# Optimization experiments

Hardware: AMD Instinct MI355X
Metric: run time of the kernel (lower is better)

Reference implementation:

```python
import jax, jax.numpy as jnp
import numpy as np

B = 64          # number of batch items (segments)
L = 16          # tokens per header unit
IS = 1024       # hidden size iS
LENS = np.arange(B, dtype=np.int32) + 32   # ragged l_hs: 32..95, sum=4064, max=95
T = int(LENS.sum())
MAXL = int(LENS.max())
EPS = 1e-12


def setup_inputs() -> dict:
    key = jax.random.key(0)
    ks = jax.random.split(key, 5)
    s_is = 1.0 / np.sqrt(IS)
    s_2is = 1.0 / np.sqrt(2 * IS)
    return {
        "ctx": jax.random.normal(ks[0], (B, IS), jnp.float32),
        "wemb_hpu": jax.random.normal(ks[1], (T, L, IS), jnp.float32),
        "l_hpu": jnp.full((T,), L, dtype=jnp.int32),   # unused by forward (kept for signature parity)
        "l_hs": jnp.asarray(LENS),
        "max_l": MAXL,
        "U_w": jax.random.normal(ks[2], (IS, IS), jnp.float32) * s_is,
        "U_b": jnp.zeros((IS,), jnp.float32),
        "V_w": jax.random.normal(ks[3], (IS, IS), jnp.float32) * s_is,
        "V_b": jnp.zeros((IS,), jnp.float32),
        "enc_w": jax.random.normal(ks[4], (IS, 2 * IS), jnp.float32) * s_2is,
        "enc_b": jnp.zeros((IS,), jnp.float32),
        "gamma": jnp.ones((IS,), jnp.float32),
        "beta": jnp.zeros((IS,), jnp.float32),
    }


def reference(ctx, wemb_hpu, l_hpu, l_hs, max_l, U_w, U_b, V_w, V_b, enc_w, enc_b, gamma, beta):
    Bn, iS = ctx.shape
    Tn = wemb_hpu.shape[0]
    # map each of the T ragged rows to its batch segment b, and its position within the segment
    seg = jnp.repeat(jnp.arange(Bn), l_hs, total_repeat_length=Tn)          # [T]
    offs = jnp.concatenate([jnp.zeros((1,), l_hs.dtype), jnp.cumsum(l_hs)[:-1]])
    pos = jnp.arange(Tn) - offs[seg]                                        # [T]

    wenc_u = ctx @ U_w.T + U_b                                              # [B, iS]
    wenc_v = wemb_hpu @ V_w.T + V_b                                         # [T, L, iS]
    # attn = softmax over L of sum_d( U(ctx)[b] * V(wenc) )
    scores = jnp.einsum('tld,td->tl', wenc_v, wenc_u[seg])                  # [T, L]
    attn = jax.nn.softmax(scores, axis=-1)
    pooled = jnp.einsum('tl,tld->td', attn, wemb_hpu)                       # [T, iS]
    h = jnp.concatenate([pooled, ctx[seg]], axis=-1) @ enc_w.T + enc_b      # [T, iS]

    # scatter ragged rows into zero-padded [B, max_l, iS]
    padded = jnp.zeros((Bn, max_l, iS), h.dtype).at[seg, pos].set(h)

    # TF-style LayerNorm over last dim (applied to padding too, as in original)
    u = padded.mean(-1, keepdims=True)
    s2 = ((padded - u) ** 2).mean(-1, keepdims=True)
    return gamma * (padded - u) / jnp.sqrt(s2 + EPS) + beta
```

## Files before the change

kernel.cpp:

```cpp
#include <hip/hip_runtime.h>

typedef unsigned short u16;
typedef unsigned int u32;
typedef __attribute__((ext_vector_type(8))) short s16x8;
typedef __attribute__((ext_vector_type(4))) float f32x4;

#define IS_ 1024
#define LTOK 16

__device__ __forceinline__ u16 f2bf(float f) {
  u32 u = __builtin_bit_cast(u32, f);
  u32 r = (u + 0x7FFFu + ((u >> 16) & 1u)) >> 16;
  return (u16)r;
}

__device__ __forceinline__ float dot4(const float4& a, const float4& b) {
  return a.x * b.x + a.y * b.y + a.z * b.z + a.w * b.w;
}

__global__ void k_pre0(const int* __restrict__ l_hs, int* __restrict__ offs,
                       int* __restrict__ seg, int Bn, int Tn, int Mp) {
  __shared__ int so[65];
  const int tid = threadIdx.x;
  if (tid < 64) {
    int v = (tid < Bn) ? l_hs[tid] : 0;
#pragma unroll
    for (int off = 1; off < 64; off <<= 1) {
      int up = __shfl_up(v, off, 64);
      if (tid >= off) v += up;
    }
    so[tid + 1] = v;
    if (tid == 0) so[0] = 0;
  }
  __syncthreads();
  if (tid < 65) offs[tid] = so[tid];
  for (int t = tid; t < Mp; t += 256) {
    int s = 0;
    if (t < Tn) {
      int lo = 0, hi = Bn;
      while (hi - lo > 1) {
        int mid = (lo + hi) >> 1;
        if (so[mid] <= t) lo = mid; else hi = mid;
      }
      s = lo;
    }
    seg[t] = s;
  }
}

__global__ __launch_bounds__(256) void k_convW1(const float* __restrict__ enc_w,
                                                u16* __restrict__ W1) {
  const int i = blockIdx.x * 1024 + threadIdx.x * 4;
  const int r = i >> 10, k = i & 1023;
  float4 v = *(const float4*)&enc_w[(size_t)r * 2048 + k];
  uint2 pk;
  pk.x = (u32)f2bf(v.x) | ((u32)f2bf(v.y) << 16);
  pk.y = (u32)f2bf(v.z) | ((u32)f2bf(v.w) << 16);
  *(uint2*)&W1[i] = pk;
}

__global__ __launch_bounds__(256) void k_rowdot(const float* __restrict__ x,
                                                const float* __restrict__ W,
                                                const float* __restrict__ bias,
                                                float* __restrict__ outp,
                                                int ldW, int colOff) {
  __shared__ float cs[2][IS_];
  const int tid = threadIdx.x;
  const int b0 = blockIdx.y * 2;
  const int d = blockIdx.x * 256 + tid;
#pragma unroll
  for (int i = 0; i < 8; ++i) {
    int idx = i * 256 + tid;
    cs[idx >> 10][idx & 1023] = x[(b0 + (idx >> 10)) * IS_ + (idx & 1023)];
  }
  __syncthreads();
  float a0 = bias[d];
  float a1 = a0;
  const float* wr = W + (size_t)d * ldW + colOff;
#pragma unroll 4
  for (int e = 0; e < IS_; e += 4) {
    float4 w4 = *(const float4*)(wr + e);
    float4 c0 = *(const float4*)&cs[0][e];
    float4 c1 = *(const float4*)&cs[1][e];
    a0 += dot4(w4, c0);
    a1 += dot4(w4, c1);
  }
  outp[b0 * IS_ + d] = a0;
  outp[(b0 + 1) * IS_ + d] = a1;
}

__global__ __launch_bounds__(256) void k_preQ(const float* __restrict__ wencu,
                                              const float* __restrict__ Vw,
                                              float* __restrict__ q2) {
  __shared__ float us[2][IS_];
  const int tid = threadIdx.x;
  const int b0 = blockIdx.y * 2;
  const int e = blockIdx.x * 256 + tid;
#pragma unroll
  for (int i = 0; i < 8; ++i) {
    int idx = i * 256 + tid;
    us[idx >> 10][idx & 1023] = wencu[(b0 + (idx >> 10)) * IS_ + (idx & 1023)];
  }
  __syncthreads();
  float a0 = 0.f, a1 = 0.f;
#pragma unroll 2
  for (int dd = 0; dd < IS_; dd += 4) {
    float4 u0 = *(const float4*)&us[0][dd];
    float4 u1 = *(const float4*)&us[1][dd];
    float v0 = Vw[(size_t)(dd + 0) * IS_ + e];
    float v1 = Vw[(size_t)(dd + 1) * IS_ + e];
    float v2 = Vw[(size_t)(dd + 2) * IS_ + e];
    float v3 = Vw[(size_t)(dd + 3) * IS_ + e];
    a0 += u0.x * v0 + u0.y * v1 + u0.z * v2 + u0.w * v3;
    a1 += u1.x * v0 + u1.y * v1 + u1.z * v2 + u1.w * v3;
  }
  q2[b0 * IS_ + e] = a0;
  q2[(b0 + 1) * IS_ + e] = a1;
}

__global__ __launch_bounds__(256) void k_attn(const float* __restrict__ wemb,
                                              const float* __restrict__ q2,
                                              const int* __restrict__ seg,
                                              u16* __restrict__ pooled, int Tn) {
  const int t = blockIdx.x;
  const int tid = threadIdx.x;
  const int d4 = tid * 4;
  if (t >= Tn) {
    uint2 z; z.x = 0u; z.y = 0u;
    *(uint2*)&pooled[(size_t)t * IS_ + d4] = z;
    return;
  }
  const int b = seg[t];
  float4 q = *(const float4*)&q2[b * IS_ + d4];
  float4 w[LTOK];
  const float* base = wemb + (size_t)t * (LTOK * IS_) + d4;
#pragma unroll
  for (int l = 0; l < LTOK; ++l) w[l] = *(const float4*)(base + l * IS_);
  float s[LTOK];
#pragma unroll
  for (int l = 0; l < LTOK; ++l) s[l] = dot4(w[l], q);
#pragma unroll
  for (int l = 0; l < LTOK; ++l) {
#pragma unroll
    for (int m = 1; m < 64; m <<= 1) s[l] += __shfl_xor(s[l], m, 64);
  }
  __shared__ float sred[4][LTOK];
  const int wave = tid >> 6, lane = tid & 63;
  if (lane == 0) {
#pragma unroll
    for (int l = 0; l < LTOK; ++l) sred[wave][l] = s[l];
  }
  __syncthreads();
  float sc[LTOK];
#pragma unroll
  for (int l = 0; l < LTOK; ++l)
    sc[l] = sred[0][l] + sred[1][l] + sred[2][l] + sred[3][l];
  float mx = sc[0];
#pragma unroll
  for (int l = 1; l < LTOK; ++l) mx = fmaxf(mx, sc[l]);
  float den = 0.f;
#pragma unroll
  for (int l = 0; l < LTOK; ++l) { sc[l] = __expf(sc[l] - mx); den += sc[l]; }
  const float inv = 1.f / den;
  float px = 0.f, py = 0.f, pz = 0.f, pw = 0.f;
#pragma unroll
  for (int l = 0; l < LTOK; ++l) {
    float a = sc[l] * inv;
    px += a * w[l].x; py += a * w[l].y; pz += a * w[l].z; pw += a * w[l].w;
  }
  uint2 pk;
  pk.x = (u32)f2bf(px) | ((u32)f2bf(py) << 16);
  pk.y = (u32)f2bf(pz) | ((u32)f2bf(pw) << 16);
  *(uint2*)&pooled[(size_t)t * IS_ + d4] = pk;
}

__device__ __forceinline__ void gl2lds16(const void* g, void* l) {
  __builtin_amdgcn_global_load_lds(
      (const __attribute__((address_space(1))) u32*)g,
      (__attribute__((address_space(3))) u32*)l, 16, 0, 0);
}

__global__ __launch_bounds__(256) void k_gemm(const u16* __restrict__ A,
                                              const u16* __restrict__ B,
                                              float* __restrict__ C) {
  __shared__ __align__(16) u16 As[128 * 64];
  __shared__ __align__(16) u16 Bs[128 * 64];
  const int tid = threadIdx.x;
  const int wave = tid >> 6, lane = tid & 63;
  const int m0 = blockIdx.x * 128, n0 = blockIdx.y * 128;
  const int wm = (wave & 1) * 64, wn = (wave >> 1) * 64;
  f32x4 acc[4][4] = {};
  for (int kt = 0; kt < 1024; kt += 64) {
#pragma unroll
    for (int c = 0; c < 4; ++c) {
      int idx = c * 256 + tid;
      int row = idx >> 3;
      int kk = (idx & 7) * 8;
      gl2lds16(A + (size_t)(m0 + row) * 1024 + kt + kk, &As[idx * 8]);
      gl2lds16(B + (size_t)(n0 + row) * 1024 + kt + kk, &Bs[idx * 8]);
    }
    __syncthreads();
#pragma unroll
    for (int ks = 0; ks < 2; ++ks) {
      const int kb = ks * 32 + (lane >> 4) * 8;
      const int rr = lane & 15;
      s16x8 af[4], bf[4];
#pragma unroll
      for (int i = 0; i < 4; ++i) {
        af[i] = *(const s16x8*)&As[(wm + i * 16 + rr) * 64 + kb];
        bf[i] = *(const s16x8*)&Bs[(wn + i * 16 + rr) * 64 + kb];
      }
#pragma unroll
      for (int i = 0; i < 4; ++i)
#pragma unroll
        for (int j = 0; j < 4; ++j)
          acc[i][j] = __builtin_amdgcn_mfma_f32_16x16x32_bf16(af[i], bf[j], acc[i][j], 0, 0, 0);
    }
    __syncthreads();
  }
  const int col = lane & 15, rq = (lane >> 4) * 4;
#pragma unroll
  for (int i = 0; i < 4; ++i)
#pragma unroll
    for (int j = 0; j < 4; ++j) {
#pragma unroll
      for (int r = 0; r < 4; ++r)
        C[(size_t)(m0 + wm + i * 16 + rq + r) * 1024 + (n0 + wn + j * 16 + col)] = acc[i][j][r];
    }
}

__global__ __launch_bounds__(256) void k_ln(const float* __restrict__ h,
                                            const float* __restrict__ h2,
                                            const int* __restrict__ offs,
                                            const int* __restrict__ l_hs,
                                            const float* __restrict__ gamma,
                                            const float* __restrict__ beta,
                                            float* __restrict__ out, int maxL) {
  const int row = blockIdx.x;
  const int b = row / maxL, pos = row % maxL;
  const int tid = threadIdx.x, d4 = tid * 4;
  float4 be = *(const float4*)&beta[d4];
  float* orow = out + (size_t)row * IS_;
  if (pos >= l_hs[b]) {
    *(float4*)(orow + d4) = be;
    return;
  }
  const int t = offs[b] + pos;
  float4 x = *(const float4*)&h[(size_t)t * IS_ + d4];
  float4 y2 = *(const float4*)&h2[b * IS_ + d4];
  x.x += y2.x; x.y += y2.y; x.z += y2.z; x.w += y2.w;
  float s1 = x.x + x.y + x.z + x.w;
  float s2 = x.x * x.x + x.y * x.y + x.z * x.z + x.w * x.w;
#pragma unroll
  for (int m = 1; m < 64; m <<= 1) {
    s1 += __shfl_xor(s1, m, 64);
    s2 += __shfl_xor(s2, m, 64);
  }
  __shared__ float red[4][2];
  const int wave = tid >> 6, lane = tid & 63;
  if (lane == 0) { red[wave][0] = s1; red[wave][1] = s2; }
  __syncthreads();
  float S1 = red[0][0] + red[1][0] + red[2][0] + red[3][0];
  float S2 = red[0][1] + red[1][1] + red[2][1] + red[3][1];
  const float u = S1 * (1.f / 1024.f);
  const float var = S2 * (1.f / 1024.f) - u * u;
  const float rstd = rsqrtf(var + 1e-12f);
  float4 g = *(const float4*)&gamma[d4];
  float4 o;
  o.x = g.x * (x.x - u) * rstd + be.x;
  o.y = g.y * (x.y - u) * rstd + be.y;
  o.z = g.z * (x.z - u) * rstd + be.z;
  o.w = g.w * (x.w - u) * rstd + be.w;
  *(float4*)(orow + d4) = o;
}

extern "C" void kernel_launch(void* const* d_in, const int* in_sizes, int n_in,
                              void* d_out, int out_size, void* d_ws, size_t ws_size,
                              hipStream_t stream) {
  const float* ctx   = (const float*)d_in[0];
  const float* wemb  = (const float*)d_in[1];
  const int*   l_hs  = (const int*)d_in[3];
  const float* U_w   = (const float*)d_in[5];
  const float* U_b   = (const float*)d_in[6];
  const float* V_w   = (const float*)d_in[7];
  const float* enc_w = (const float*)d_in[9];
  const float* enc_b = (const float*)d_in[10];
  const float* gamma = (const float*)d_in[11];
  const float* beta  = (const float*)d_in[12];
  float* out = (float*)d_out;

  const int Bn = in_sizes[0] / IS_;
  const int Tn = in_sizes[1] / (LTOK * IS_);
  const int maxL = out_size / (Bn * IS_);
  const int Mp = (Tn + 127) & ~127;

  char* ws = (char*)d_ws;
  int*   offs   = (int*)(ws + 0x0);
  int*   seg    = (int*)(ws + 0x400);
  float* wencu  = (float*)(ws + 0x10000);
  float* q2     = (float*)(ws + 0x50000);
  float* h2     = (float*)(ws + 0x90000);
  u16*   W1     = (u16*)(ws + 0xD0000);
  u16*   pooled = (u16*)(ws + 0x2D0000);
  float* h      = (float*)(ws + 0xAD0000);

  k_pre0<<<1, 256, 0, stream>>>(l_hs, offs, seg, Bn, Tn, Mp);
  k_convW1<<<1024, 256, 0, stream>>>(enc_w, W1);
  k_rowdot<<<dim3(4, Bn / 2), 256, 0, stream>>>(ctx, U_w, U_b, wencu, 1024, 0);
  k_rowdot<<<dim3(4, Bn / 2), 256, 0, stream>>>(ctx, enc_w, enc_b, h2, 2048, 1024);
  k_preQ<<<dim3(4, Bn / 2), 256, 0, stream>>>(wencu, V_w, q2);
  k_attn<<<Mp, 256, 0, stream>>>(wemb, q2, seg, pooled, Tn);
  k_gemm<<<dim3(Mp / 128, 8), 256, 0, stream>>>(pooled, W1, h);
  k_ln<<<Bn * maxL, 256, 0, stream>>>(h, h2, offs, l_hs, gamma, beta, out, maxL);
}
```

Before: 593.6 us.

## Merge prep kernels, retile small ctx matvecs with split-K, butterfly score reduction

Folds the segment-offset prep into the weight conversion kernel and merges the two ctx row-dot launches into one split-K kernel that processes 8 batch rows per block. The q2 projection is retiled to 4 batch rows per block with a 4-way split-K, and k_attn replaces 16 separate full wave reductions with a transpose-style butterfly that reduces all 16 scores using fewer shuffles. The goal is fewer launches, more weight reuse per load in the small matvecs, and less shuffle work in attention. It adds shared-memory partial-sum reductions and lane-permutation index logic.

```diff
diff --git a/kernel.cpp b/kernel.cpp
--- a/kernel.cpp
+++ b/kernel.cpp
@@ -18,39 +18,41 @@
   return a.x * b.x + a.y * b.y + a.z * b.z + a.w * b.w;
 }
 
-__global__ void k_pre0(const int* __restrict__ l_hs, int* __restrict__ offs,
-                       int* __restrict__ seg, int Bn, int Tn, int Mp) {
-  __shared__ int so[65];
-  const int tid = threadIdx.x;
-  if (tid < 64) {
-    int v = (tid < Bn) ? l_hs[tid] : 0;
-#pragma unroll
-    for (int off = 1; off < 64; off <<= 1) {
-      int up = __shfl_up(v, off, 64);
-      if (tid >= off) v += up;
-    }
-    so[tid + 1] = v;
-    if (tid == 0) so[0] = 0;
-  }
-  __syncthreads();
-  if (tid < 65) offs[tid] = so[tid];
-  for (int t = tid; t < Mp; t += 256) {
-    int s = 0;
-    if (t < Tn) {
-      int lo = 0, hi = Bn;
-      while (hi - lo > 1) {
-        int mid = (lo + hi) >> 1;
-        if (so[mid] <= t) lo = mid; else hi = mid;
+__global__ __launch_bounds__(256) void k_prep(const float* __restrict__ enc_w,
+                                              u16* __restrict__ W1,
+                                              const int* __restrict__ l_hs,
+                                              int* __restrict__ offs,
+                                              int* __restrict__ seg,
+                                              int Bn, int Tn, int Mp) {
+  const int tid = threadIdx.x;
+  if (blockIdx.x == 0) {
+    __shared__ int so[65];
+    if (tid < 64) {
+      int v = (tid < Bn) ? l_hs[tid] : 0;
+#pragma unroll
+      for (int off = 1; off < 64; off <<= 1) {
+        int up = __shfl_up(v, off, 64);
+        if (tid >= off) v += up;
       }
-      s = lo;
-    }
-    seg[t] = s;
-  }
-}
-
-__global__ __launch_bounds__(256) void k_convW1(const float* __restrict__ enc_w,
-                                                u16* __restrict__ W1) {
-  const int i = blockIdx.x * 1024 + threadIdx.x * 4;
+      so[tid + 1] = v;
+      if (tid == 0) so[0] = 0;
+    }
+    __syncthreads();
+    if (tid < 65) offs[tid] = so[tid];
+    for (int t = tid; t < Mp; t += 256) {
+      int s = 0;
+      if (t < Tn) {
+        int lo = 0, hi = Bn;
+        while (hi - lo > 1) {
+          int mid = (lo + hi) >> 1;
+          if (so[mid] <= t) lo = mid; else hi = mid;
+        }
+        s = lo;
+      }
+      seg[t] = s;
+    }
+  }
+  const int i = blockIdx.x * 1024 + tid * 4;
   const int r = i >> 10, k = i & 1023;
   float4 v = *(const float4*)&enc_w[(size_t)r * 2048 + k];
   uint2 pk;
@@ -59,63 +61,88 @@
   *(uint2*)&W1[i] = pk;
 }
 
-__global__ __launch_bounds__(256) void k_rowdot(const float* __restrict__ x,
-                                                const float* __restrict__ W,
-                                                const float* __restrict__ bias,
-                                                float* __restrict__ outp,
-                                                int ldW, int colOff) {
-  __shared__ float cs[2][IS_];
-  const int tid = threadIdx.x;
-  const int b0 = blockIdx.y * 2;
-  const int d = blockIdx.x * 256 + tid;
-#pragma unroll
-  for (int i = 0; i < 8; ++i) {
-    int idx = i * 256 + tid;
-    cs[idx >> 10][idx & 1023] = x[(b0 + (idx >> 10)) * IS_ + (idx & 1023)];
-  }
-  __syncthreads();
-  float a0 = bias[d];
-  float a1 = a0;
-  const float* wr = W + (size_t)d * ldW + colOff;
+__global__ __launch_bounds__(256) void k_ctxmm(const float* __restrict__ ctx,
+                                               const float* __restrict__ U_w,
+                                               const float* __restrict__ U_b,
+                                               const float* __restrict__ enc_w,
+                                               const float* __restrict__ enc_b,
+                                               float* __restrict__ wencu,
+                                               float* __restrict__ h2) {
+  const int z = blockIdx.z;
+  const float* W = z ? enc_w : U_w;
+  const float* bias = z ? enc_b : U_b;
+  float* outp = z ? h2 : wencu;
+  const int ldW = z ? 2048 : 1024;
+  const int colOff = z ? 1024 : 0;
+  const int d0 = blockIdx.x * 64;
+  const int b0 = blockIdx.y * 8;
+  const int tid = threadIdx.x;
+  const int dl = tid & 63;
+  const int ks = tid >> 6;
+  __shared__ float xs[8][IS_];
+  __shared__ float rs[4][64][8];
+#pragma unroll
+  for (int it = 0; it < 8; ++it) {
+    int i = it * 256 + tid;
+    int bb = i >> 8, kk = (i & 255) * 4;
+    *(float4*)&xs[bb][kk] = *(const float4*)&ctx[(size_t)(b0 + bb) * IS_ + kk];
+  }
+  __syncthreads();
+  const float* wr = W + (size_t)(d0 + dl) * ldW + colOff + ks * 256;
+  float acc[8] = {0, 0, 0, 0, 0, 0, 0, 0};
 #pragma unroll 4
-  for (int e = 0; e < IS_; e += 4) {
-    float4 w4 = *(const float4*)(wr + e);
-    float4 c0 = *(const float4*)&cs[0][e];
-    float4 c1 = *(const float4*)&cs[1][e];
-    a0 += dot4(w4, c0);
-    a1 += dot4(w4, c1);
-  }
-  outp[b0 * IS_ + d] = a0;
-  outp[(b0 + 1) * IS_ + d] = a1;
-}
-
-__global__ __launch_bounds__(256) void k_preQ(const float* __restrict__ wencu,
-                                              const float* __restrict__ Vw,
-                                              float* __restrict__ q2) {
-  __shared__ float us[2][IS_];
-  const int tid = threadIdx.x;
-  const int b0 = blockIdx.y * 2;
-  const int e = blockIdx.x * 256 + tid;
-#pragma unroll
-  for (int i = 0; i < 8; ++i) {
-    int idx = i * 256 + tid;
-    us[idx >> 10][idx & 1023] = wencu[(b0 + (idx >> 10)) * IS_ + (idx & 1023)];
-  }
-  __syncthreads();
-  float a0 = 0.f, a1 = 0.f;
-#pragma unroll 2
-  for (int dd = 0; dd < IS_; dd += 4) {
-    float4 u0 = *(const float4*)&us[0][dd];
-    float4 u1 = *(const float4*)&us[1][dd];
-    float v0 = Vw[(size_t)(dd + 0) * IS_ + e];
-    float v1 = Vw[(size_t)(dd + 1) * IS_ + e];
-    float v2 = Vw[(size_t)(dd + 2) * IS_ + e];
-    float v3 = Vw[(size_t)(dd + 3) * IS_ + e];
-    a0 += u0.x * v0 + u0.y * v1 + u0.z * v2 + u0.w * v3;
-    a1 += u1.x * v0 + u1.y * v1 + u1.z * v2 + u1.w * v3;
-  }
-  q2[b0 * IS_ + e] = a0;
-  q2[(b0 + 1) * IS_ + e] = a1;
+  for (int k = 0; k < 256; k += 4) {
+    float4 w4 = *(const float4*)(wr + k);
+#pragma unroll
+    for (int b = 0; b < 8; ++b) {
+      float4 x4 = *(const float4*)&xs[b][ks * 256 + k];
+      acc[b] += dot4(w4, x4);
+    }
+  }
+#pragma unroll
+  for (int b = 0; b < 8; ++b) rs[ks][dl][b] = acc[b];
+  __syncthreads();
+#pragma unroll
+  for (int rep = 0; rep < 2; ++rep) {
+    int o = rep * 256 + tid;
+    int dd = o >> 3, bb = o & 7;
+    float v = bias[d0 + dd] + rs[0][dd][bb] + rs[1][dd][bb] + rs[2][dd][bb] + rs[3][dd][bb];
+    outp[(size_t)(b0 + bb) * IS_ + d0 + dd] = v;
+  }
+}
+
+__global__ __launch_bounds__(256) void k_q2(const float* __restrict__ wencu,
+                                            const float* __restrict__ Vw,
+                                            float* __restrict__ q2) {
+  const int e0 = blockIdx.x * 64;
+  const int b0 = blockIdx.y * 4;
+  const int tid = threadIdx.x;
+  const int el = tid & 63;
+  const int ks = tid >> 6;
+  __shared__ float xs[4][IS_];
+  __shared__ float rs[4][64][4];
+#pragma unroll
+  for (int it = 0; it < 4; ++it) {
+    int i = it * 256 + tid;
+    int bb = i >> 8, kk = (i & 255) * 4;
+    *(float4*)&xs[bb][kk] = *(const float4*)&wencu[(size_t)(b0 + bb) * IS_ + kk];
+  }
+  __syncthreads();
+  const int dbase = ks * 256;
+  float acc[4] = {0, 0, 0, 0};
+#pragma unroll 4
+  for (int d = 0; d < 256; ++d) {
+    float v = Vw[(size_t)(dbase + d) * IS_ + e0 + el];
+#pragma unroll
+    for (int b = 0; b < 4; ++b) acc[b] += xs[b][dbase + d] * v;
+  }
+#pragma unroll
+  for (int b = 0; b < 4; ++b) rs[ks][el][b] = acc[b];
+  __syncthreads();
+  int o = tid;
+  int ee = o >> 2, bb = o & 3;
+  float v = rs[0][ee][bb] + rs[1][ee][bb] + rs[2][ee][bb] + rs[3][ee][bb];
+  q2[(size_t)(b0 + bb) * IS_ + e0 + ee] = v;
 }
 
 __global__ __launch_bounds__(256) void k_attn(const float* __restrict__ wemb,
@@ -139,16 +166,26 @@
   float s[LTOK];
 #pragma unroll
   for (int l = 0; l < LTOK; ++l) s[l] = dot4(w[l], q);
-#pragma unroll
-  for (int l = 0; l < LTOK; ++l) {
-#pragma unroll
-    for (int m = 1; m < 64; m <<= 1) s[l] += __shfl_xor(s[l], m, 64);
-  }
+  const int wave = tid >> 6, lane = tid & 63;
+#pragma unroll
+  for (int m = 1; m <= 8; m <<= 1) {
+    const int live = 16 / m;
+    const int half = live >> 1;
+    const bool hi = (lane & m) != 0;
+#pragma unroll
+    for (int i = 0; i < half; ++i) {
+      float tosend = hi ? s[i] : s[i + half];
+      float recv = __shfl_xor(tosend, m, 64);
+      float keep = hi ? s[i + half] : s[i];
+      s[i] = keep + recv;
+    }
+  }
+  s[0] += __shfl_xor(s[0], 16, 64);
+  s[0] += __shfl_xor(s[0], 32, 64);
   __shared__ float sred[4][LTOK];
-  const int wave = tid >> 6, lane = tid & 63;
-  if (lane == 0) {
-#pragma unroll
-    for (int l = 0; l < LTOK; ++l) sred[wave][l] = s[l];
+  if (lane < 16) {
+    int v = ((lane & 1) << 3) | ((lane & 2) << 1) | ((lane & 4) >> 1) | ((lane & 8) >> 3);
+    sred[wave][v] = s[0];
   }
   __syncthreads();
   float sc[LTOK];
@@ -304,11 +341,9 @@
   u16*   pooled = (u16*)(ws + 0x2D0000);
   float* h      = (float*)(ws + 0xAD0000);
 
-  k_pre0<<<1, 256, 0, stream>>>(l_hs, offs, seg, Bn, Tn, Mp);
-  k_convW1<<<1024, 256, 0, stream>>>(enc_w, W1);
-  k_rowdot<<<dim3(4, Bn / 2), 256, 0, stream>>>(ctx, U_w, U_b, wencu, 1024, 0);
-  k_rowdot<<<dim3(4, Bn / 2), 256, 0, stream>>>(ctx, enc_w, enc_b, h2, 2048, 1024);
-  k_preQ<<<dim3(4, Bn / 2), 256, 0, stream>>>(wencu, V_w, q2);
+  k_prep<<<1024, 256, 0, stream>>>(enc_w, W1, l_hs, offs, seg, Bn, Tn, Mp);
+  k_ctxmm<<<dim3(16, Bn / 8, 2), 256, 0, stream>>>(ctx, U_w, U_b, enc_w, enc_b, wencu, h2);
+  k_q2<<<dim3(16, Bn / 4), 256, 0, stream>>>(wencu, V_w, q2);
   k_attn<<<Mp, 256, 0, stream>>>(wemb, q2, seg, pooled, Tn);
   k_gemm<<<dim3(Mp / 128, 8), 256, 0, stream>>>(pooled, W1, h);
   k_ln<<<Bn * maxL, 256, 0, stream>>>(h, h2, offs, l_hs, gamma, beta, out, maxL);
```

Measured after the change: 498.9 us. -15.9%, faster.
